# Optimization experiments

Measured on AMD Instinct MI355X. Metric: run time of the kernel, lower is better.

The kernel has to match this reference:

```python
import jax, jax.numpy as jnp
import numpy as np

ROUTED_SCALING_FACTOR = 2.5


def setup_inputs() -> dict:
    key = jax.random.key(0)
    k1, k2, k3 = jax.random.split(key, 3)
    tokens, hidden, n_experts = 16384, 7168, 256
    x = jax.random.normal(k1, (tokens, hidden), dtype=jnp.float32)
    gate_weight = jax.random.normal(k2, (n_experts, hidden), dtype=jnp.float32) * 0.02
    e_score_correction_bias = jax.random.normal(k3, (n_experts,), dtype=jnp.float32) * 0.1
    return {
        "x": x,
        "gate_weight": gate_weight,
        "e_score_correction_bias": e_score_correction_bias,
        "top_k": 8,
    }


def reference(x, gate_weight, e_score_correction_bias, top_k):
    # logits: [tokens, n_experts]
    logits = jnp.einsum("th,eh->te", x.astype(jnp.float32), gate_weight.astype(jnp.float32))
    scores = jax.nn.sigmoid(logits)
    scores_with_bias = scores + e_score_correction_bias  # bias only affects selection
    # sorted top-k over experts (lax.top_k returns sorted descending)
    _, topk_indices = jax.lax.top_k(scores_with_bias, top_k)
    topk_scores = jnp.take_along_axis(scores, topk_indices, axis=-1)  # [tokens, top_k]
    scores_sum = jnp.sum(topk_scores, axis=-1, keepdims=True) + 1e-20
    topk_weights = topk_scores / scores_sum * ROUTED_SCALING_FACTOR
    return (topk_indices, topk_weights)
```

## Files before the change

kernel.cpp:

```cpp
#include <hip/hip_runtime.h>
#include <hip/hip_bf16.h>
#include <math.h>

#define M_TOK 16384
#define N_EXP 256
#define K_DIM 7168
#define BM 64
#define BK 32
#define KSTEPS (K_DIM / BK)
#define KH (KSTEPS / 2)
#define WTILE 32768
#define IMG_BYTES ((size_t)KSTEPS * WTILE)
#define P_ELEMS ((size_t)M_TOK * N_EXP)
#define TOPK 8
#define SX 4096.0f
#define SW 16384.0f
#define DESCALE 1.4901161193847656e-08f

typedef __attribute__((ext_vector_type(8))) _Float16 half8;
typedef __attribute__((ext_vector_type(4))) _Float16 half4;
typedef __attribute__((ext_vector_type(4))) float f32x4;

__device__ __forceinline__ void cvt8_2(const float* v, half8& h, half8& l) {
#pragma unroll
  for (int i = 0; i < 8; ++i) {
    _Float16 a = (_Float16)v[i];
    float r = v[i] - (float)a;
    h[i] = a;
    l[i] = (_Float16)r;
  }
}
__device__ __forceinline__ void cvt4_2(const float* v, half4& h, half4& l) {
#pragma unroll
  for (int i = 0; i < 4; ++i) {
    _Float16 a = (_Float16)v[i];
    float r = v[i] - (float)a;
    h[i] = a;
    l[i] = (_Float16)r;
  }
}

__device__ __forceinline__ unsigned long long pack_ci(float key, int idx) {
  unsigned int u = __builtin_bit_cast(unsigned int, key);
  u = (u & 0x80000000u) ? ~u : (u | 0x80000000u);
  return ((unsigned long long)u << 32) | (unsigned)(255 - idx);
}
__device__ __forceinline__ unsigned long long shflx64(unsigned long long v, int off) {
  int lo = __shfl_xor((int)(unsigned)(v & 0xffffffffull), off);
  int hi = __shfl_xor((int)(unsigned)(v >> 32), off);
  return ((unsigned long long)(unsigned)hi << 32) | (unsigned)lo;
}

__global__ void prep_w_kernel(const float* __restrict__ W, unsigned char* __restrict__ ws) {
  int t = blockIdx.x;
  int e = threadIdx.x;
  const float* src = W + (size_t)e * K_DIM + t * BK;
  unsigned char* dst = ws + (size_t)t * WTILE;
#pragma unroll
  for (int kc = 0; kc < 4; ++kc) {
    float v[8];
    float4 a = ((const float4*)src)[kc * 2];
    float4 b = ((const float4*)src)[kc * 2 + 1];
    v[0] = a.x * SW; v[1] = a.y * SW; v[2] = a.z * SW; v[3] = a.w * SW;
    v[4] = b.x * SW; v[5] = b.y * SW; v[6] = b.z * SW; v[7] = b.w * SW;
    half8 h, l;
    cvt8_2(v, h, l);
    int col = (kc * 16) ^ ((e & 6) << 3);
    *(half8*)(dst + e * 64 + col) = h;
    *(half8*)(dst + 16384 + e * 64 + col) = l;
  }
}

__global__ __launch_bounds__(512, 4) void gate_split_kernel(
    const float* __restrict__ X,
    const unsigned char* __restrict__ ws,
    float* __restrict__ part) {
  __shared__ unsigned char smem[81920] __attribute__((aligned(16)));

  const int g = blockIdx.x;
  const int khalf = (g >> 2) & 1;
  const int mtile = ((g >> 3) << 2) | (g & 3);
  const int m0 = mtile * BM;

  const int tid = threadIdx.x;
  const int lane = tid & 63;
  const int wid = tid >> 6;
  const int wm = wid >> 2;
  const int wn = wid & 3;
  const int lr = lane & 15;
  const int lg = lane >> 4;

  const unsigned char* img0 = ws + (size_t)khalf * KH * WTILE;

  int aOff[2], bOff[4];
#pragma unroll
  for (int m = 0; m < 2; ++m) {
    int r = wm * 32 + m * 16 + lr;
    aOff[m] = r * 64 + ((lg * 16) ^ ((r & 6) << 3));
  }
#pragma unroll
  for (int n = 0; n < 4; ++n) {
    int e = wn * 64 + n * 16 + lr;
    bOff[n] = e * 64 + ((lg * 16) ^ ((e & 6) << 3));
  }

  const int xr = tid >> 3;
  const int xkc = tid & 7;
  const float* xsrc = X + (size_t)(m0 + xr) * K_DIM + (size_t)khalf * KH * BK + xkc * 4;
  const int xcol = (xkc * 8) ^ ((xr & 6) << 3);

  auto load_x = [&](int t, f32x4& dst) {
    dst = __builtin_nontemporal_load((const f32x4*)(xsrc + (size_t)t * BK));
  };
  auto write_x = [&](int b, const f32x4& xv) {
    float v[4] = {xv[0] * SX, xv[1] * SX, xv[2] * SX, xv[3] * SX};
    half4 h, l;
    cvt4_2(v, h, l);
    unsigned char* Ab = smem + b * 8192;
    *(half4*)(Ab + xr * 64 + xcol) = h;
    *(half4*)(Ab + 4096 + xr * 64 + xcol) = l;
  };
  auto stage_w = [&](int t, int b) {
    unsigned char* Bb = smem + 16384 + b * 32768;
    const unsigned char* src = img0 + (size_t)t * WTILE;
#pragma unroll
    for (int i = 0; i < 4; ++i) {
      int off = i * 8192 + tid * 16;
      __builtin_amdgcn_global_load_lds(
          (const __attribute__((address_space(1))) void*)(src + off),
          (__attribute__((address_space(3))) void*)(Bb + off), 16, 0, 0);
    }
  };

  f32x4 acc[2][4];
  f32x4 accc[2][4];
#pragma unroll
  for (int m = 0; m < 2; ++m)
#pragma unroll
    for (int n = 0; n < 4; ++n) {
      acc[m][n] = (f32x4){0.f, 0.f, 0.f, 0.f};
      accc[m][n] = (f32x4){0.f, 0.f, 0.f, 0.f};
    }

  auto body = [&](int t, f32x4& xload, const f32x4& xcons) {
    const int cur = t & 1, nxt = cur ^ 1;
    if (t + 1 < KH) stage_w(t + 1, nxt);
    if (t + 2 < KH) load_x(t + 2, xload);

    const unsigned char* Ab = smem + cur * 8192;
    const unsigned char* Bb = smem + 16384 + cur * 32768;
    half8 xh[2], xl[2], wh[4], wl[4];
#pragma unroll
    for (int m = 0; m < 2; ++m) {
      xh[m] = *(const half8*)(Ab + aOff[m]);
      xl[m] = *(const half8*)(Ab + 4096 + aOff[m]);
    }
#pragma unroll
    for (int n = 0; n < 4; ++n) {
      wh[n] = *(const half8*)(Bb + bOff[n]);
      wl[n] = *(const half8*)(Bb + 16384 + bOff[n]);
    }
#pragma unroll
    for (int m = 0; m < 2; ++m)
#pragma unroll
      for (int n = 0; n < 4; ++n) {
        acc[m][n] = __builtin_amdgcn_mfma_f32_16x16x32_f16(xh[m], wh[n], acc[m][n], 0, 0, 0);
        f32x4 c = accc[m][n];
        c = __builtin_amdgcn_mfma_f32_16x16x32_f16(xh[m], wl[n], c, 0, 0, 0);
        c = __builtin_amdgcn_mfma_f32_16x16x32_f16(xl[m], wh[n], c, 0, 0, 0);
        accc[m][n] = c;
      }

    if (t + 1 < KH) {
      write_x(nxt, xcons);
      if (t + 2 < KH) {
        asm volatile("s_waitcnt vmcnt(1)" ::: "memory");
      } else {
        asm volatile("s_waitcnt vmcnt(0)" ::: "memory");
      }
      asm volatile("s_waitcnt lgkmcnt(0)" ::: "memory");
      __builtin_amdgcn_s_barrier();
    }
  };

  f32x4 xqA, xqB;
  stage_w(0, 0);
  load_x(0, xqA);
  write_x(0, xqA);
  load_x(1, xqB);
  __syncthreads();

#pragma clang loop unroll(disable)
  for (int t = 0; t < KH; t += 2) {
    body(t, xqA, xqB);
    body(t + 1, xqB, xqA);
  }

  float* dst = part + (size_t)khalf * P_ELEMS;
#pragma unroll
  for (int m = 0; m < 2; ++m)
#pragma unroll
    for (int n = 0; n < 4; ++n)
#pragma unroll
      for (int r = 0; r < 4; ++r) {
        int row = wm * 32 + m * 16 + lg * 4 + r;
        int col = wn * 64 + n * 16 + lr;
        __builtin_nontemporal_store(acc[m][n][r] + accc[m][n][r],
                                    &dst[(size_t)(m0 + row) * N_EXP + col]);
      }
}

__global__ __launch_bounds__(256) void reduce_topk_kernel(
    const float* __restrict__ part,
    const float* __restrict__ bias,
    float* __restrict__ out) {
  __shared__ float sc[32 * 260];

  const int tid = threadIdx.x;
  const int lane = tid & 63;
  const int wid = tid >> 6;
  const int r0 = blockIdx.x * 32;

  const float* p0 = part;
  const float* p1 = part + P_ELEMS;

  {
    int row = tid >> 3, seg = tid & 7;
    size_t base = (size_t)(r0 + row) * N_EXP + seg * 32;
#pragma unroll
    for (int j = 0; j < 8; ++j) {
      f32x4 a = __builtin_nontemporal_load((const f32x4*)(p0 + base + j * 4));
      f32x4 b = __builtin_nontemporal_load((const f32x4*)(p1 + base + j * 4));
#pragma unroll
      for (int e = 0; e < 4; ++e) {
        float v = (a[e] + b[e]) * DESCALE;
        sc[row * 260 + seg * 32 + j * 4 + e] = 1.0f / (1.0f + expf(-v));
      }
    }
  }
  __syncthreads();

  const float bb0 = bias[lane];
  const float bb1 = bias[lane + 64];
  const float bb2 = bias[lane + 128];
  const float bb3 = bias[lane + 192];
  const size_t TOT = (size_t)M_TOK * TOPK;

  for (int i = 0; i < 8; ++i) {
    int row = wid * 8 + i;
    float s0 = sc[row * 260 + lane];
    float s1 = sc[row * 260 + lane + 64];
    float s2 = sc[row * 260 + lane + 128];
    float s3 = sc[row * 260 + lane + 192];
    unsigned long long c0 = pack_ci(s0 + bb0, lane);
    unsigned long long c1 = pack_ci(s1 + bb1, lane + 64);
    unsigned long long c2 = pack_ci(s2 + bb2, lane + 128);
    unsigned long long c3 = pack_ci(s3 + bb3, lane + 192);
    float ssum = 0.f, my_s = 0.f;
    int my_idx = 0;
#pragma unroll
    for (int p = 0; p < TOPK; ++p) {
      unsigned long long b01 = c0 > c1 ? c0 : c1;
      unsigned long long b23 = c2 > c3 ? c2 : c3;
      unsigned long long best = b01 > b23 ? b01 : b23;
#pragma unroll
      for (int off = 1; off < 64; off <<= 1) {
        unsigned long long o = shflx64(best, off);
        if (o > best) best = o;
      }
      int idxw = 255 - (int)(best & 0xffull);
      int lw = idxw & 63;
      int jw = idxw >> 6;
      float sel = jw == 0 ? s0 : jw == 1 ? s1 : jw == 2 ? s2 : s3;
      float sw = __shfl(sel, lw);
      ssum += sw;
      if (lane == p) { my_idx = idxw; my_s = sw; }
      if (lane == lw) {
        if (jw == 0) c0 = 0ull;
        else if (jw == 1) c1 = 0ull;
        else if (jw == 2) c2 = 0ull;
        else c3 = 0ull;
      }
    }
    if (lane < TOPK) {
      size_t rg = (size_t)(r0 + row);
      out[rg * TOPK + lane] = (float)my_idx;
      out[TOT + rg * TOPK + lane] = my_s * (2.5f / (ssum + 1e-20f));
    }
  }
}

__global__ __launch_bounds__(512, 2) void gate_mono_kernel(
    const float* __restrict__ X,
    const float* __restrict__ Wg,
    const float* __restrict__ bias,
    float* __restrict__ out) {
  __shared__ unsigned char smem[81920] __attribute__((aligned(16)));

  const int tid = threadIdx.x;
  const int lane = tid & 63;
  const int wid = tid >> 6;
  const int wm = wid >> 2;
  const int wn = wid & 3;
  const int lr = lane & 15;
  const int lg = lane >> 4;
  const int m0 = blockIdx.x * BM;

  int aOff[2], bOff[4];
#pragma unroll
  for (int m = 0; m < 2; ++m) {
    int r = wm * 32 + m * 16 + lr;
    aOff[m] = r * 64 + ((lg * 16) ^ ((r & 6) << 3));
  }
#pragma unroll
  for (int n = 0; n < 4; ++n) {
    int e = wn * 64 + n * 16 + lr;
    bOff[n] = e * 64 + ((lg * 16) ^ ((e & 6) << 3));
  }

  const int xr = tid >> 3;
  const int xkc = tid & 7;
  const float* xsrc = X + (size_t)(m0 + xr) * K_DIM + xkc * 4;
  const int xcol = (xkc * 8) ^ ((xr & 6) << 3);

  auto load_x = [&](int t, f32x4& dst) {
    dst = *(const f32x4*)(xsrc + (size_t)t * BK);
  };
  auto write_x = [&](int b, const f32x4& xv) {
    float v[4] = {xv[0] * SX, xv[1] * SX, xv[2] * SX, xv[3] * SX};
    half4 h, l;
    cvt4_2(v, h, l);
    unsigned char* Ab = smem + b * 8192;
    *(half4*)(Ab + xr * 64 + xcol) = h;
    *(half4*)(Ab + 4096 + xr * 64 + xcol) = l;
  };
  auto stage_w = [&](int t, int b) {
    unsigned char* Bb = smem + 16384 + b * 32768;
    int row = tid >> 1;
    int g0 = (tid & 1) * 2;
    const float* src = Wg + (size_t)row * K_DIM + (size_t)t * BK + g0 * 8;
#pragma unroll
    for (int g = 0; g < 2; ++g) {
      float v[8];
      float4 a = ((const float4*)src)[g * 2];
      float4 bq = ((const float4*)src)[g * 2 + 1];
      v[0] = a.x * SW; v[1] = a.y * SW; v[2] = a.z * SW; v[3] = a.w * SW;
      v[4] = bq.x * SW; v[5] = bq.y * SW; v[6] = bq.z * SW; v[7] = bq.w * SW;
      half8 h, l;
      cvt8_2(v, h, l);
      int col = ((g0 + g) * 16) ^ ((row & 6) << 3);
      *(half8*)(Bb + row * 64 + col) = h;
      *(half8*)(Bb + 16384 + row * 64 + col) = l;
    }
  };

  f32x4 acc[2][4], accc[2][4];
#pragma unroll
  for (int m = 0; m < 2; ++m)
#pragma unroll
    for (int n = 0; n < 4; ++n) {
      acc[m][n] = (f32x4){0.f, 0.f, 0.f, 0.f};
      accc[m][n] = (f32x4){0.f, 0.f, 0.f, 0.f};
    }

  f32x4 xqA, xqB;
  stage_w(0, 0);
  load_x(0, xqA);
  write_x(0, xqA);
  load_x(1, xqB);
  __syncthreads();

#pragma clang loop unroll(disable)
  for (int t = 0; t < KSTEPS; ++t) {
    const int cur = t & 1, nxt = cur ^ 1;
    f32x4& xload = (t & 1) ? xqB : xqA;
    const f32x4& xcons = (t & 1) ? xqA : xqB;
    if (t + 1 < KSTEPS) stage_w(t + 1, nxt);
    if (t + 2 < KSTEPS) load_x(t + 2, xload);

    const unsigned char* Ab = smem + cur * 8192;
    const unsigned char* Bb = smem + 16384 + cur * 32768;
    half8 xh[2], xl[2], wh[4], wl[4];
#pragma unroll
    for (int m = 0; m < 2; ++m) {
      xh[m] = *(const half8*)(Ab + aOff[m]);
      xl[m] = *(const half8*)(Ab + 2048 * 2 + aOff[m]);
    }
#pragma unroll
    for (int n = 0; n < 4; ++n) {
      wh[n] = *(const half8*)(Bb + bOff[n]);
      wl[n] = *(const half8*)(Bb + 16384 + bOff[n]);
    }
#pragma unroll
    for (int m = 0; m < 2; ++m)
#pragma unroll
      for (int n = 0; n < 4; ++n) {
        acc[m][n] = __builtin_amdgcn_mfma_f32_16x16x32_f16(xh[m], wh[n], acc[m][n], 0, 0, 0);
        f32x4 c = accc[m][n];
        c = __builtin_amdgcn_mfma_f32_16x16x32_f16(xh[m], wl[n], c, 0, 0, 0);
        c = __builtin_amdgcn_mfma_f32_16x16x32_f16(xl[m], wh[n], c, 0, 0, 0);
        accc[m][n] = c;
      }
    if (t + 1 < KSTEPS) {
      write_x(nxt, xcons);
      __syncthreads();
    }
  }
  __syncthreads();

  float* sc = (float*)smem;
#pragma unroll
  for (int m = 0; m < 2; ++m)
#pragma unroll
    for (int n = 0; n < 4; ++n)
#pragma unroll
      for (int r = 0; r < 4; ++r) {
        int row = wm * 32 + m * 16 + lg * 4 + r;
        int col = wn * 64 + n * 16 + lr;
        float v = (acc[m][n][r] + accc[m][n][r]) * DESCALE;
        sc[row * 260 + col] = 1.0f / (1.0f + expf(-v));
      }
  __syncthreads();

  const float bb0 = bias[lane];
  const float bb1 = bias[lane + 64];
  const float bb2 = bias[lane + 128];
  const float bb3 = bias[lane + 192];
  const size_t TOT = (size_t)M_TOK * TOPK;

  for (int i = 0; i < 8; ++i) {
    int row = wid * 8 + i;
    float s0 = sc[row * 260 + lane];
    float s1 = sc[row * 260 + lane + 64];
    float s2 = sc[row * 260 + lane + 128];
    float s3 = sc[row * 260 + lane + 192];
    unsigned long long c0 = pack_ci(s0 + bb0, lane);
    unsigned long long c1 = pack_ci(s1 + bb1, lane + 64);
    unsigned long long c2 = pack_ci(s2 + bb2, lane + 128);
    unsigned long long c3 = pack_ci(s3 + bb3, lane + 192);
    float ssum = 0.f, my_s = 0.f;
    int my_idx = 0;
#pragma unroll
    for (int p = 0; p < TOPK; ++p) {
      unsigned long long b01 = c0 > c1 ? c0 : c1;
      unsigned long long b23 = c2 > c3 ? c2 : c3;
      unsigned long long best = b01 > b23 ? b01 : b23;
#pragma unroll
      for (int off = 1; off < 64; off <<= 1) {
        unsigned long long o = shflx64(best, off);
        if (o > best) best = o;
      }
      int idxw = 255 - (int)(best & 0xffull);
      int lw = idxw & 63;
      int jw = idxw >> 6;
      float sel = jw == 0 ? s0 : jw == 1 ? s1 : jw == 2 ? s2 : s3;
      float sw = __shfl(sel, lw);
      ssum += sw;
      if (lane == p) { my_idx = idxw; my_s = sw; }
      if (lane == lw) {
        if (jw == 0) c0 = 0ull;
        else if (jw == 1) c1 = 0ull;
        else if (jw == 2) c2 = 0ull;
        else c3 = 0ull;
      }
    }
    if (lane < TOPK) {
      size_t rg = (size_t)(m0 + row);
      out[rg * TOPK + lane] = (float)my_idx;
      out[TOT + rg * TOPK + lane] = my_s * (2.5f / (ssum + 1e-20f));
    }
  }
}

extern "C" void kernel_launch(void* const* d_in, const int* in_sizes, int n_in,
                              void* d_out, int out_size, void* d_ws, size_t ws_size,
                              hipStream_t stream) {
  const float* X = (const float*)d_in[0];
  const float* W = (const float*)d_in[1];
  const float* bias = (const float*)d_in[2];
  float* out = (float*)d_out;

  const size_t need = IMG_BYTES + 2 * P_ELEMS * sizeof(float);
  if (d_ws != nullptr && ws_size >= need) {
    unsigned char* ws = (unsigned char*)d_ws;
    float* part = (float*)(ws + IMG_BYTES);
    prep_w_kernel<<<KSTEPS, 256, 0, stream>>>(W, ws);
    gate_split_kernel<<<2 * (M_TOK / BM), 512, 0, stream>>>(X, ws, part);
    reduce_topk_kernel<<<M_TOK / 32, 256, 0, stream>>>(part, bias, out);
  } else {
    gate_mono_kernel<<<M_TOK / BM, 512, 0, stream>>>(X, W, bias, out);
  }
}
```

Measured before the change: 260.0 us.

## Read weight fragments straight from global memory and shrink split-K GEMM blocks

The split-K gate GEMM kernel no longer stages the pre-converted weight image into LDS. Each wave now loads its own 64-expert weight fragments directly from global memory (and L2) into registers. Block size drops from 512 to 256 threads and the M tile from 64 to 32 tokens, so LDS use falls to 8 KB for the X tile only. MFMA clusters are wrapped in s_setprio and sched_barrier to interleave them with the split weight loads. This is meant to remove LDS weight-staging traffic and raise occupancy, at the cost of more redundant global and L2 weight reads per token row and exposed global-load latency inside the loop.

```diff
diff --git a/kernel.cpp b/kernel.cpp
--- a/kernel.cpp
+++ b/kernel.cpp
@@ -5,7 +5,6 @@
 #define M_TOK 16384
 #define N_EXP 256
 #define K_DIM 7168
-#define BM 64
 #define BK 32
 #define KSTEPS (K_DIM / BK)
 #define KH (KSTEPS / 2)
@@ -71,37 +70,32 @@
   }
 }
 
-__global__ __launch_bounds__(512, 4) void gate_split_kernel(
+__global__ __launch_bounds__(256, 4) void gate_split_kernel(
     const float* __restrict__ X,
     const unsigned char* __restrict__ ws,
     float* __restrict__ part) {
-  __shared__ unsigned char smem[81920] __attribute__((aligned(16)));
+  __shared__ unsigned char smem[8192] __attribute__((aligned(16)));
 
   const int g = blockIdx.x;
   const int khalf = (g >> 2) & 1;
   const int mtile = ((g >> 3) << 2) | (g & 3);
-  const int m0 = mtile * BM;
+  const int m0 = mtile * 32;
 
   const int tid = threadIdx.x;
   const int lane = tid & 63;
   const int wid = tid >> 6;
-  const int wm = wid >> 2;
-  const int wn = wid & 3;
   const int lr = lane & 15;
   const int lg = lane >> 4;
 
-  const unsigned char* img0 = ws + (size_t)khalf * KH * WTILE;
-
-  int aOff[2], bOff[4];
-#pragma unroll
-  for (int m = 0; m < 2; ++m) {
-    int r = wm * 32 + m * 16 + lr;
-    aOff[m] = r * 64 + ((lg * 16) ^ ((r & 6) << 3));
-  }
-#pragma unroll
-  for (int n = 0; n < 4; ++n) {
-    int e = wn * 64 + n * 16 + lr;
-    bOff[n] = e * 64 + ((lg * 16) ^ ((e & 6) << 3));
+  const int wOff = (wid * 64 + lr) * 64 + ((lg * 16) ^ ((lr & 6) << 3));
+  const unsigned char* wH = ws + (size_t)khalf * KH * WTILE + wOff;
+  const unsigned char* wL = wH + 16384;
+
+  int aOff0, aOff1;
+  {
+    int r0 = lr, r1 = 16 + lr;
+    aOff0 = r0 * 64 + ((lg * 16) ^ ((r0 & 6) << 3));
+    aOff1 = r1 * 64 + ((lg * 16) ^ ((r1 & 6) << 3));
   }
 
   const int xr = tid >> 3;
@@ -109,27 +103,13 @@
   const float* xsrc = X + (size_t)(m0 + xr) * K_DIM + (size_t)khalf * KH * BK + xkc * 4;
   const int xcol = (xkc * 8) ^ ((xr & 6) << 3);
 
-  auto load_x = [&](int t, f32x4& dst) {
-    dst = __builtin_nontemporal_load((const f32x4*)(xsrc + (size_t)t * BK));
-  };
   auto write_x = [&](int b, const f32x4& xv) {
     float v[4] = {xv[0] * SX, xv[1] * SX, xv[2] * SX, xv[3] * SX};
     half4 h, l;
     cvt4_2(v, h, l);
-    unsigned char* Ab = smem + b * 8192;
+    unsigned char* Ab = smem + b * 4096;
     *(half4*)(Ab + xr * 64 + xcol) = h;
-    *(half4*)(Ab + 4096 + xr * 64 + xcol) = l;
-  };
-  auto stage_w = [&](int t, int b) {
-    unsigned char* Bb = smem + 16384 + b * 32768;
-    const unsigned char* src = img0 + (size_t)t * WTILE;
-#pragma unroll
-    for (int i = 0; i < 4; ++i) {
-      int off = i * 8192 + tid * 16;
-      __builtin_amdgcn_global_load_lds(
-          (const __attribute__((address_space(1))) void*)(src + off),
-          (__attribute__((address_space(3))) void*)(Bb + off), 16, 0, 0);
-    }
+    *(half4*)(Ab + 2048 + xr * 64 + xcol) = l;
   };
 
   f32x4 acc[2][4];
@@ -142,59 +122,68 @@
       accc[m][n] = (f32x4){0.f, 0.f, 0.f, 0.f};
     }
 
-  auto body = [&](int t, f32x4& xload, const f32x4& xcons) {
-    const int cur = t & 1, nxt = cur ^ 1;
-    if (t + 1 < KH) stage_w(t + 1, nxt);
-    if (t + 2 < KH) load_x(t + 2, xload);
-
-    const unsigned char* Ab = smem + cur * 8192;
-    const unsigned char* Bb = smem + 16384 + cur * 32768;
-    half8 xh[2], xl[2], wh[4], wl[4];
-#pragma unroll
-    for (int m = 0; m < 2; ++m) {
-      xh[m] = *(const half8*)(Ab + aOff[m]);
-      xl[m] = *(const half8*)(Ab + 4096 + aOff[m]);
-    }
-#pragma unroll
-    for (int n = 0; n < 4; ++n) {
-      wh[n] = *(const half8*)(Bb + bOff[n]);
-      wl[n] = *(const half8*)(Bb + 16384 + bOff[n]);
-    }
-#pragma unroll
-    for (int m = 0; m < 2; ++m)
-#pragma unroll
-      for (int n = 0; n < 4; ++n) {
-        acc[m][n] = __builtin_amdgcn_mfma_f32_16x16x32_f16(xh[m], wh[n], acc[m][n], 0, 0, 0);
-        f32x4 c = accc[m][n];
-        c = __builtin_amdgcn_mfma_f32_16x16x32_f16(xh[m], wl[n], c, 0, 0, 0);
-        c = __builtin_amdgcn_mfma_f32_16x16x32_f16(xl[m], wh[n], c, 0, 0, 0);
-        accc[m][n] = c;
-      }
-
-    if (t + 1 < KH) {
-      write_x(nxt, xcons);
-      if (t + 2 < KH) {
-        asm volatile("s_waitcnt vmcnt(1)" ::: "memory");
-      } else {
-        asm volatile("s_waitcnt vmcnt(0)" ::: "memory");
-      }
+#define CLUSTER(N, WH, WL)                                                        \
+  acc[0][N] = __builtin_amdgcn_mfma_f32_16x16x32_f16(xh0, WH, acc[0][N], 0, 0, 0); \
+  acc[1][N] = __builtin_amdgcn_mfma_f32_16x16x32_f16(xh1, WH, acc[1][N], 0, 0, 0); \
+  accc[0][N] = __builtin_amdgcn_mfma_f32_16x16x32_f16(xl0, WH, accc[0][N], 0, 0, 0); \
+  accc[1][N] = __builtin_amdgcn_mfma_f32_16x16x32_f16(xl1, WH, accc[1][N], 0, 0, 0); \
+  accc[0][N] = __builtin_amdgcn_mfma_f32_16x16x32_f16(xh0, WL, accc[0][N], 0, 0, 0); \
+  accc[1][N] = __builtin_amdgcn_mfma_f32_16x16x32_f16(xh1, WL, accc[1][N], 0, 0, 0);
+
+  auto body = [&](int t, int cur) {
+    f32x4 xq;
+    const bool hasNext = (t + 1 < KH);
+    if (hasNext)
+      xq = __builtin_nontemporal_load((const f32x4*)(xsrc + (size_t)(t + 1) * BK));
+
+    const unsigned char* wpH = wH + (size_t)t * WTILE;
+    const unsigned char* wpL = wL + (size_t)t * WTILE;
+    half8 wh0 = *(const half8*)(wpH);
+    half8 wh1 = *(const half8*)(wpH + 1024);
+    half8 wl0 = *(const half8*)(wpL);
+    half8 wl1 = *(const half8*)(wpL + 1024);
+
+    const unsigned char* Ab = smem + cur * 4096;
+    half8 xh0 = *(const half8*)(Ab + aOff0);
+    half8 xh1 = *(const half8*)(Ab + aOff1);
+    half8 xl0 = *(const half8*)(Ab + 2048 + aOff0);
+    half8 xl1 = *(const half8*)(Ab + 2048 + aOff1);
+
+    __builtin_amdgcn_s_setprio(1);
+    CLUSTER(0, wh0, wl0)
+    CLUSTER(1, wh1, wl1)
+    __builtin_amdgcn_s_setprio(0);
+    __builtin_amdgcn_sched_barrier(0);
+
+    half8 wh2 = *(const half8*)(wpH + 2048);
+    half8 wh3 = *(const half8*)(wpH + 3072);
+    half8 wl2 = *(const half8*)(wpL + 2048);
+    half8 wl3 = *(const half8*)(wpL + 3072);
+
+    __builtin_amdgcn_s_setprio(1);
+    CLUSTER(2, wh2, wl2)
+    CLUSTER(3, wh3, wl3)
+    __builtin_amdgcn_s_setprio(0);
+
+    if (hasNext) {
+      write_x(cur ^ 1, xq);
       asm volatile("s_waitcnt lgkmcnt(0)" ::: "memory");
       __builtin_amdgcn_s_barrier();
     }
   };
 
-  f32x4 xqA, xqB;
-  stage_w(0, 0);
-  load_x(0, xqA);
-  write_x(0, xqA);
-  load_x(1, xqB);
-  __syncthreads();
+  {
+    f32x4 x0 = __builtin_nontemporal_load((const f32x4*)xsrc);
+    write_x(0, x0);
+    __syncthreads();
+  }
 
 #pragma clang loop unroll(disable)
   for (int t = 0; t < KH; t += 2) {
-    body(t, xqA, xqB);
-    body(t + 1, xqB, xqA);
-  }
+    body(t, 0);
+    body(t + 1, 1);
+  }
+#undef CLUSTER
 
   float* dst = part + (size_t)khalf * P_ELEMS;
 #pragma unroll
@@ -203,8 +192,8 @@
     for (int n = 0; n < 4; ++n)
 #pragma unroll
       for (int r = 0; r < 4; ++r) {
-        int row = wm * 32 + m * 16 + lg * 4 + r;
-        int col = wn * 64 + n * 16 + lr;
+        int row = m * 16 + lg * 4 + r;
+        int col = wid * 64 + n * 16 + lr;
         __builtin_nontemporal_store(acc[m][n][r] + accc[m][n][r],
                                     &dst[(size_t)(m0 + row) * N_EXP + col]);
       }
@@ -304,7 +293,7 @@
   const int wn = wid & 3;
   const int lr = lane & 15;
   const int lg = lane >> 4;
-  const int m0 = blockIdx.x * BM;
+  const int m0 = blockIdx.x * 64;
 
   int aOff[2], bOff[4];
 #pragma unroll
@@ -384,7 +373,7 @@
 #pragma unroll
     for (int m = 0; m < 2; ++m) {
       xh[m] = *(const half8*)(Ab + aOff[m]);
-      xl[m] = *(const half8*)(Ab + 2048 * 2 + aOff[m]);
+      xl[m] = *(const half8*)(Ab + 4096 + aOff[m]);
     }
 #pragma unroll
     for (int n = 0; n < 4; ++n) {
@@ -485,9 +474,9 @@
     unsigned char* ws = (unsigned char*)d_ws;
     float* part = (float*)(ws + IMG_BYTES);
     prep_w_kernel<<<KSTEPS, 256, 0, stream>>>(W, ws);
-    gate_split_kernel<<<2 * (M_TOK / BM), 512, 0, stream>>>(X, ws, part);
+    gate_split_kernel<<<2 * (M_TOK / 32), 256, 0, stream>>>(X, ws, part);
     reduce_topk_kernel<<<M_TOK / 32, 256, 0, stream>>>(part, bias, out);
   } else {
-    gate_mono_kernel<<<M_TOK / BM, 512, 0, stream>>>(X, W, bias, out);
-  }
-}
+    gate_mono_kernel<<<M_TOK / 64, 512, 0, stream>>>(X, W, bias, out);
+  }
+}
```

After: 313.1 us. +20.4%, slower.

## Enlarge split GEMM M-tile to 128 and read weights directly from global into registers

Applied to the files above, without the earlier changes.

The split-K gate GEMM now uses 128-row tiles, with each warp covering 64 rows, and reads the preformatted fp16 weight image straight from global memory into registers instead of staging it through LDS with global_load_lds. Only X is double-buffered in shared memory, which cuts LDS use to 32KB, and the launch bound drops to 2 blocks per CU. Each weight fragment is reused across twice as many rows, and the LDS traffic and wait for weight staging go away. In exchange, weight loads are no longer prefetched a step ahead, so their latency may be exposed, and more accumulator registers are needed.

```diff
diff --git a/kernel.cpp b/kernel.cpp
--- a/kernel.cpp
+++ b/kernel.cpp
@@ -5,7 +5,6 @@
 #define M_TOK 16384
 #define N_EXP 256
 #define K_DIM 7168
-#define BM 64
 #define BK 32
 #define KSTEPS (K_DIM / BK)
 #define KH (KSTEPS / 2)
@@ -71,16 +70,15 @@
   }
 }
 
-__global__ __launch_bounds__(512, 4) void gate_split_kernel(
+__global__ __launch_bounds__(512, 2) void gate_split_kernel(
     const float* __restrict__ X,
     const unsigned char* __restrict__ ws,
     float* __restrict__ part) {
-  __shared__ unsigned char smem[81920] __attribute__((aligned(16)));
+  __shared__ unsigned char smem[32768] __attribute__((aligned(16)));
 
   const int g = blockIdx.x;
-  const int khalf = (g >> 2) & 1;
-  const int mtile = ((g >> 3) << 2) | (g & 3);
-  const int m0 = mtile * BM;
+  const int khalf = g & 1;
+  const int m0 = (g >> 1) * 128;
 
   const int tid = threadIdx.x;
   const int lane = tid & 63;
@@ -91,122 +89,98 @@
   const int lg = lane >> 4;
 
   const unsigned char* img0 = ws + (size_t)khalf * KH * WTILE;
-
-  int aOff[2], bOff[4];
-#pragma unroll
-  for (int m = 0; m < 2; ++m) {
-    int r = wm * 32 + m * 16 + lr;
+  const int wOff = (wn * 64 + lr) * 64 + ((lg * 16) ^ ((lr & 6) << 3));
+
+  int aOff[4];
+#pragma unroll
+  for (int m = 0; m < 4; ++m) {
+    int r = wm * 64 + m * 16 + lr;
     aOff[m] = r * 64 + ((lg * 16) ^ ((r & 6) << 3));
   }
-#pragma unroll
-  for (int n = 0; n < 4; ++n) {
-    int e = wn * 64 + n * 16 + lr;
-    bOff[n] = e * 64 + ((lg * 16) ^ ((e & 6) << 3));
-  }
-
-  const int xr = tid >> 3;
-  const int xkc = tid & 7;
-  const float* xsrc = X + (size_t)(m0 + xr) * K_DIM + (size_t)khalf * KH * BK + xkc * 4;
-  const int xcol = (xkc * 8) ^ ((xr & 6) << 3);
-
-  auto load_x = [&](int t, f32x4& dst) {
-    dst = __builtin_nontemporal_load((const f32x4*)(xsrc + (size_t)t * BK));
+
+  const int xr = tid >> 2;
+  const int xkc = tid & 3;
+  const float* xsrc = X + (size_t)(m0 + xr) * K_DIM + (size_t)khalf * KH * BK + xkc * 8;
+  const int xcol = (xkc * 16) ^ ((xr & 6) << 3);
+
+  auto write_x = [&](int b, const f32x4& x0, const f32x4& x1) {
+    float v[8] = {x0[0] * SX, x0[1] * SX, x0[2] * SX, x0[3] * SX,
+                  x1[0] * SX, x1[1] * SX, x1[2] * SX, x1[3] * SX};
+    half8 h, l;
+    cvt8_2(v, h, l);
+    unsigned char* Ab = smem + b * 16384;
+    *(half8*)(Ab + xr * 64 + xcol) = h;
+    *(half8*)(Ab + 8192 + xr * 64 + xcol) = l;
   };
-  auto write_x = [&](int b, const f32x4& xv) {
-    float v[4] = {xv[0] * SX, xv[1] * SX, xv[2] * SX, xv[3] * SX};
-    half4 h, l;
-    cvt4_2(v, h, l);
-    unsigned char* Ab = smem + b * 8192;
-    *(half4*)(Ab + xr * 64 + xcol) = h;
-    *(half4*)(Ab + 4096 + xr * 64 + xcol) = l;
-  };
-  auto stage_w = [&](int t, int b) {
-    unsigned char* Bb = smem + 16384 + b * 32768;
-    const unsigned char* src = img0 + (size_t)t * WTILE;
-#pragma unroll
-    for (int i = 0; i < 4; ++i) {
-      int off = i * 8192 + tid * 16;
-      __builtin_amdgcn_global_load_lds(
-          (const __attribute__((address_space(1))) void*)(src + off),
-          (__attribute__((address_space(3))) void*)(Bb + off), 16, 0, 0);
-    }
-  };
-
-  f32x4 acc[2][4];
-  f32x4 accc[2][4];
-#pragma unroll
-  for (int m = 0; m < 2; ++m)
+
+  f32x4 acc[4][4];
+  f32x4 accc[4][4];
+#pragma unroll
+  for (int m = 0; m < 4; ++m)
 #pragma unroll
     for (int n = 0; n < 4; ++n) {
       acc[m][n] = (f32x4){0.f, 0.f, 0.f, 0.f};
       accc[m][n] = (f32x4){0.f, 0.f, 0.f, 0.f};
     }
 
-  auto body = [&](int t, f32x4& xload, const f32x4& xcons) {
-    const int cur = t & 1, nxt = cur ^ 1;
-    if (t + 1 < KH) stage_w(t + 1, nxt);
-    if (t + 2 < KH) load_x(t + 2, xload);
-
-    const unsigned char* Ab = smem + cur * 8192;
-    const unsigned char* Bb = smem + 16384 + cur * 32768;
-    half8 xh[2], xl[2], wh[4], wl[4];
-#pragma unroll
-    for (int m = 0; m < 2; ++m) {
-      xh[m] = *(const half8*)(Ab + aOff[m]);
-      xl[m] = *(const half8*)(Ab + 4096 + aOff[m]);
-    }
-#pragma unroll
-    for (int n = 0; n < 4; ++n) {
-      wh[n] = *(const half8*)(Bb + bOff[n]);
-      wl[n] = *(const half8*)(Bb + 16384 + bOff[n]);
-    }
-#pragma unroll
-    for (int m = 0; m < 2; ++m)
+  {
+    f32x4 x0 = __builtin_nontemporal_load((const f32x4*)xsrc);
+    f32x4 x1 = __builtin_nontemporal_load((const f32x4*)(xsrc + 4));
+    write_x(0, x0, x1);
+    __syncthreads();
+  }
+
+#pragma clang loop unroll(disable)
+  for (int t = 0; t < KH; ++t) {
+    const int cur = t & 1;
+    const bool hasNext = (t + 1 < KH);
+
+    f32x4 xq0, xq1;
+    if (hasNext) {
+      xq0 = __builtin_nontemporal_load((const f32x4*)(xsrc + (size_t)(t + 1) * BK));
+      xq1 = __builtin_nontemporal_load((const f32x4*)(xsrc + (size_t)(t + 1) * BK + 4));
+    }
+
+    const unsigned char* wp = img0 + (size_t)t * WTILE + wOff;
+    half8 wh[4], wl[4];
+#pragma unroll
+    for (int n = 0; n < 4; ++n) wh[n] = *(const half8*)(wp + n * 1024);
+#pragma unroll
+    for (int n = 0; n < 4; ++n) wl[n] = *(const half8*)(wp + 16384 + n * 1024);
+
+    const unsigned char* Ab = smem + cur * 16384;
+#pragma unroll
+    for (int m = 0; m < 4; ++m) {
+      half8 xh = *(const half8*)(Ab + aOff[m]);
+      half8 xl = *(const half8*)(Ab + 8192 + aOff[m]);
 #pragma unroll
       for (int n = 0; n < 4; ++n) {
-        acc[m][n] = __builtin_amdgcn_mfma_f32_16x16x32_f16(xh[m], wh[n], acc[m][n], 0, 0, 0);
+        acc[m][n] = __builtin_amdgcn_mfma_f32_16x16x32_f16(xh, wh[n], acc[m][n], 0, 0, 0);
         f32x4 c = accc[m][n];
-        c = __builtin_amdgcn_mfma_f32_16x16x32_f16(xh[m], wl[n], c, 0, 0, 0);
-        c = __builtin_amdgcn_mfma_f32_16x16x32_f16(xl[m], wh[n], c, 0, 0, 0);
+        c = __builtin_amdgcn_mfma_f32_16x16x32_f16(xl, wh[n], c, 0, 0, 0);
+        c = __builtin_amdgcn_mfma_f32_16x16x32_f16(xh, wl[n], c, 0, 0, 0);
         accc[m][n] = c;
       }
-
-    if (t + 1 < KH) {
-      write_x(nxt, xcons);
-      if (t + 2 < KH) {
-        asm volatile("s_waitcnt vmcnt(1)" ::: "memory");
-      } else {
-        asm volatile("s_waitcnt vmcnt(0)" ::: "memory");
-      }
+    }
+
+    if (hasNext) {
+      write_x(cur ^ 1, xq0, xq1);
       asm volatile("s_waitcnt lgkmcnt(0)" ::: "memory");
       __builtin_amdgcn_s_barrier();
     }
-  };
-
-  f32x4 xqA, xqB;
-  stage_w(0, 0);
-  load_x(0, xqA);
-  write_x(0, xqA);
-  load_x(1, xqB);
-  __syncthreads();
-
-#pragma clang loop unroll(disable)
-  for (int t = 0; t < KH; t += 2) {
-    body(t, xqA, xqB);
-    body(t + 1, xqB, xqA);
-  }
-
-  float* dst = part + (size_t)khalf * P_ELEMS;
-#pragma unroll
-  for (int m = 0; m < 2; ++m)
+  }
+
+  float* dst = part + (size_t)khalf * P_ELEMS + (size_t)m0 * N_EXP;
+#pragma unroll
+  for (int m = 0; m < 4; ++m)
 #pragma unroll
     for (int n = 0; n < 4; ++n)
 #pragma unroll
       for (int r = 0; r < 4; ++r) {
-        int row = wm * 32 + m * 16 + lg * 4 + r;
+        int row = wm * 64 + m * 16 + lg * 4 + r;
         int col = wn * 64 + n * 16 + lr;
         __builtin_nontemporal_store(acc[m][n][r] + accc[m][n][r],
-                                    &dst[(size_t)(m0 + row) * N_EXP + col]);
+                                    &dst[(size_t)row * N_EXP + col]);
       }
 }
 
@@ -304,7 +278,7 @@
   const int wn = wid & 3;
   const int lr = lane & 15;
   const int lg = lane >> 4;
-  const int m0 = blockIdx.x * BM;
+  const int m0 = blockIdx.x * 64;
 
   int aOff[2], bOff[4];
 #pragma unroll
@@ -384,7 +358,7 @@
 #pragma unroll
     for (int m = 0; m < 2; ++m) {
       xh[m] = *(const half8*)(Ab + aOff[m]);
-      xl[m] = *(const half8*)(Ab + 2048 * 2 + aOff[m]);
+      xl[m] = *(const half8*)(Ab + 4096 + aOff[m]);
     }
 #pragma unroll
     for (int n = 0; n < 4; ++n) {
@@ -485,9 +459,9 @@
     unsigned char* ws = (unsigned char*)d_ws;
     float* part = (float*)(ws + IMG_BYTES);
     prep_w_kernel<<<KSTEPS, 256, 0, stream>>>(W, ws);
-    gate_split_kernel<<<2 * (M_TOK / BM), 512, 0, stream>>>(X, ws, part);
+    gate_split_kernel<<<2 * (M_TOK / 128), 512, 0, stream>>>(X, ws, part);
     reduce_topk_kernel<<<M_TOK / 32, 256, 0, stream>>>(part, bias, out);
   } else {
-    gate_mono_kernel<<<M_TOK / BM, 512, 0, stream>>>(X, W, bias, out);
-  }
-}
+    gate_mono_kernel<<<M_TOK / 64, 512, 0, stream>>>(X, W, bias, out);
+  }
+}
```

After: 306.2 us. 1.18x slower.
